# Optimization experiments

Measured on AMD Instinct MI355X. Metric: run time of the kernel, lower is better.

Reference implementation:

```python
import jax, jax.numpy as jnp
import numpy as np

N_NODES = 100000
D_NODE = 80
N_EDGES = 1600000


def setup_inputs() -> dict:
    key = jax.random.key(0)
    ks = jax.random.split(key, 8)
    nodeEmbed = jax.random.normal(ks[0], (N_NODES, D_NODE), dtype=jnp.float32)
    edge_index = jax.random.randint(ks[1], (2, N_EDGES), 0, N_NODES, dtype=jnp.int32)
    # Linear params (fan-in scaled)
    W1 = jax.random.normal(ks[2], (161, 32), dtype=jnp.float32) / np.sqrt(161.0)
    b1 = jax.random.normal(ks[3], (32,), dtype=jnp.float32) * 0.01
    W2 = jax.random.normal(ks[4], (32, 32), dtype=jnp.float32) / np.sqrt(32.0)
    b2 = jax.random.normal(ks[5], (32,), dtype=jnp.float32) * 0.01
    W3 = jax.random.normal(ks[6], (32, 2), dtype=jnp.float32) / np.sqrt(32.0)
    b3 = jax.random.normal(ks[7], (2,), dtype=jnp.float32) * 0.01
    return {"nodeEmbed": nodeEmbed, "edge_index": edge_index,
            "W1": W1, "b1": b1, "W2": W2, "b2": b2, "W3": W3, "b3": b3}


def reference(nodeEmbed, edge_index, W1, b1, W2, b2, W3, b3):
    # embedEdges: gather src/dst node embeddings, concat with constant edge feat
    x_src = nodeEmbed[edge_index[0]]          # [E, 80]
    x_dst = nodeEmbed[edge_index[1]]          # [E, 80]
    edge_feats = jnp.ones((edge_index.shape[1], 1), dtype=nodeEmbed.dtype)
    edge_embed = jnp.concatenate([x_src, edge_feats, x_dst], axis=-1)  # [E, 161]
    # forward: lin1 -> relu -> lin2 -> relu -> lin3 -> log_softmax
    h = jax.nn.relu(edge_embed @ W1 + b1)     # [E, 32]
    h = jax.nn.relu(h @ W2 + b2)              # [E, 32]
    logits = h @ W3 + b3                      # [E, 2]
    return jax.nn.log_softmax(logits, axis=1)
```

## Files before the change

### kernel.cpp

```cpp
#include <hip/hip_runtime.h>
#include <hip/hip_bf16.h>

#define D_NODE 80
#define EDGE_ITERS 8

typedef __attribute__((ext_vector_type(8))) short short8;
typedef __attribute__((ext_vector_type(16))) float f32x16;

__device__ __forceinline__ float bf16lo(unsigned u) {
    return __uint_as_float(u << 16);
}
__device__ __forceinline__ float bf16hi(unsigned u) {
    return __uint_as_float(u & 0xffff0000u);
}
__device__ __forceinline__ unsigned packbf2(float a, float b) {
    __hip_bfloat162 h = __float22bfloat162_rn(make_float2(a, b));
    union { __hip_bfloat162 h2; unsigned u; } cv; cv.h2 = h;
    return cv.u;
}
__device__ __forceinline__ short f2bf(float f) {
    __hip_bfloat16 h = __float2bfloat16(f);
    union { __hip_bfloat16 h1; short s; } cv; cv.h1 = h;
    return cv.s;
}

__global__ __launch_bounds__(256) void proj_kernel(
    const float* __restrict__ X, const float* __restrict__ W1,
    const float* __restrict__ b1,
    unsigned short* __restrict__ PS, unsigned short* __restrict__ PD, int N)
{
    const int lane = threadIdx.x & 63;
    const int wave = threadIdx.x >> 6;
    const int n    = lane & 31;
    const int hi   = lane >> 5;

    short8 Ws[5], Wd[5];
#pragma unroll
    for (int s = 0; s < 5; ++s) {
#pragma unroll
        for (int j = 0; j < 8; ++j) {
            int k = s * 16 + hi * 8 + j;
            Ws[s][j] = f2bf(W1[k * 32 + n]);
            Wd[s][j] = f2bf(W1[(81 + k) * 32 + n]);
        }
    }
    float cdInit[16];
#pragma unroll
    for (int r = 0; r < 16; ++r) {
        int f = (r & 3) + 8 * (r >> 2) + 4 * hi;
        cdInit[r] = b1[f] + W1[80 * 32 + f];
    }

    const int tiles = N / 32;
    for (int tile = blockIdx.x * 4 + wave; tile < tiles; tile += gridDim.x * 4) {
        const int node = tile * 32 + n;
        const float4* xrow = (const float4*)(X + (size_t)node * D_NODE + hi * 8);

        f32x16 cs, cd;
#pragma unroll
        for (int r = 0; r < 16; ++r) { cs[r] = 0.0f; cd[r] = cdInit[r]; }

#pragma unroll
        for (int s = 0; s < 5; ++s) {
            float4 xa = xrow[s * 4];
            float4 xb = xrow[s * 4 + 1];
            union { uint4 u; short8 s8; } Bx;
            Bx.u.x = packbf2(xa.x, xa.y);
            Bx.u.y = packbf2(xa.z, xa.w);
            Bx.u.z = packbf2(xb.x, xb.y);
            Bx.u.w = packbf2(xb.z, xb.w);
            cs = __builtin_amdgcn_mfma_f32_32x32x16_bf16(Ws[s], Bx.s8, cs, 0, 0, 0);
            cd = __builtin_amdgcn_mfma_f32_32x32x16_bf16(Wd[s], Bx.s8, cd, 0, 0, 0);
        }

        unsigned short* psr = PS + (size_t)node * 32 + hi * 4;
        unsigned short* pdr = PD + (size_t)node * 32 + hi * 4;
#pragma unroll
        for (int q = 0; q < 4; ++q) {
            uint2 vs = make_uint2(packbf2(cs[4*q+0], cs[4*q+1]),
                                  packbf2(cs[4*q+2], cs[4*q+3]));
            uint2 vd = make_uint2(packbf2(cd[4*q+0], cd[4*q+1]),
                                  packbf2(cd[4*q+2], cd[4*q+3]));
            *(uint2*)(psr + q * 8) = vs;
            *(uint2*)(pdr + q * 8) = vd;
        }
    }
}

__global__ __launch_bounds__(256) void edge_kernel(
    const int* __restrict__ ei,
    const unsigned short* __restrict__ PS, const unsigned short* __restrict__ PD,
    const float* __restrict__ W2, const float* __restrict__ b2,
    const float* __restrict__ W3, const float* __restrict__ b3,
    float* __restrict__ out, int E)
{
    const int tid  = threadIdx.x;
    const int wave = tid >> 6;
    const int lane = tid & 63;
    const int n    = lane & 31;
    const int hi   = lane >> 5;

    short8 Wa0, Wa1;
#pragma unroll
    for (int j = 0; j < 8; ++j) {
        int k0 = hi * 8 + j;
        Wa0[j] = f2bf(W2[k0 * 32 + n]);
        Wa1[j] = f2bf(W2[(16 + k0) * 32 + n]);
    }
    unsigned b2p[8], w3p[16];
#pragma unroll
    for (int r = 0; r < 16; ++r) {
        int row = (r & 3) + 8 * (r >> 2) + 4 * hi;
        w3p[r] = packbf2(W3[row * 2 + 0], W3[row * 2 + 1]);
        if ((r & 1) == 0) {
            int row2 = ((r + 1) & 3) + 8 * ((r + 1) >> 2) + 4 * hi;
            b2p[r >> 1] = packbf2(b2[row], b2[row2]);
        }
    }
    const float b30 = b3[0], b31 = b3[1];

    const long base = ((long)blockIdx.x * 4 + wave) * (32 * EDGE_ITERS);

    int sIdx[EDGE_ITERS], dIdx[EDGE_ITERS];
#pragma unroll
    for (int it = 0; it < EDGE_ITERS; ++it) {
        long e = base + (long)it * 32 + n;
        int ec = (e < E) ? (int)e : 0;
        sIdx[it] = ei[ec];
        dIdx[it] = ei[(size_t)E + ec];
    }

    uint4 av0 = *(const uint4*)(PS + (size_t)sIdx[0] * 32 + hi * 8);
    uint4 av1 = *(const uint4*)(PS + (size_t)sIdx[0] * 32 + 16 + hi * 8);
    uint4 bv0 = *(const uint4*)(PD + (size_t)dIdx[0] * 32 + hi * 8);
    uint4 bv1 = *(const uint4*)(PD + (size_t)dIdx[0] * 32 + 16 + hi * 8);

#pragma unroll
    for (int it = 0; it < EDGE_ITERS; ++it) {
        uint4 pav0, pav1, pbv0, pbv1;
        if (it + 1 < EDGE_ITERS) {
            pav0 = *(const uint4*)(PS + (size_t)sIdx[it+1] * 32 + hi * 8);
            pav1 = *(const uint4*)(PS + (size_t)sIdx[it+1] * 32 + 16 + hi * 8);
            pbv0 = *(const uint4*)(PD + (size_t)dIdx[it+1] * 32 + hi * 8);
            pbv1 = *(const uint4*)(PD + (size_t)dIdx[it+1] * 32 + 16 + hi * 8);
        }

        union { uint4 u; short8 s8; } B0, B1;
        B0.u.x = packbf2(fmaxf(bf16lo(av0.x) + bf16lo(bv0.x), 0.f),
                         fmaxf(bf16hi(av0.x) + bf16hi(bv0.x), 0.f));
        B0.u.y = packbf2(fmaxf(bf16lo(av0.y) + bf16lo(bv0.y), 0.f),
                         fmaxf(bf16hi(av0.y) + bf16hi(bv0.y), 0.f));
        B0.u.z = packbf2(fmaxf(bf16lo(av0.z) + bf16lo(bv0.z), 0.f),
                         fmaxf(bf16hi(av0.z) + bf16hi(bv0.z), 0.f));
        B0.u.w = packbf2(fmaxf(bf16lo(av0.w) + bf16lo(bv0.w), 0.f),
                         fmaxf(bf16hi(av0.w) + bf16hi(bv0.w), 0.f));
        B1.u.x = packbf2(fmaxf(bf16lo(av1.x) + bf16lo(bv1.x), 0.f),
                         fmaxf(bf16hi(av1.x) + bf16hi(bv1.x), 0.f));
        B1.u.y = packbf2(fmaxf(bf16lo(av1.y) + bf16lo(bv1.y), 0.f),
                         fmaxf(bf16hi(av1.y) + bf16hi(bv1.y), 0.f));
        B1.u.z = packbf2(fmaxf(bf16lo(av1.z) + bf16lo(bv1.z), 0.f),
                         fmaxf(bf16hi(av1.z) + bf16hi(bv1.z), 0.f));
        B1.u.w = packbf2(fmaxf(bf16lo(av1.w) + bf16lo(bv1.w), 0.f),
                         fmaxf(bf16hi(av1.w) + bf16hi(bv1.w), 0.f));

        f32x16 c;
#pragma unroll
        for (int q = 0; q < 8; ++q) {
            c[2*q]   = bf16lo(b2p[q]);
            c[2*q+1] = bf16hi(b2p[q]);
        }
        c = __builtin_amdgcn_mfma_f32_32x32x16_bf16(Wa0, B0.s8, c, 0, 0, 0);
        c = __builtin_amdgcn_mfma_f32_32x32x16_bf16(Wa1, B1.s8, c, 0, 0, 0);

        float p0 = 0.f, p1 = 0.f;
#pragma unroll
        for (int r = 0; r < 16; ++r) {
            float h = fmaxf(c[r], 0.f);
            p0 += h * bf16lo(w3p[r]);
            p1 += h * bf16hi(w3p[r]);
        }
        p0 += __shfl_xor(p0, 32, 64);
        p1 += __shfl_xor(p1, 32, 64);

        if (hi == 0) {
            long eo = base + (long)it * 32 + n;
            if (eo < E) {
                float l0 = p0 + b30;
                float l1 = p1 + b31;
                float mm = fmaxf(l0, l1);
                float z  = __expf(l0 - mm) + __expf(l1 - mm);
                float lse = mm + __logf(z);
                *(float2*)(out + 2 * eo) = make_float2(l0 - lse, l1 - lse);
            }
        }
        av0 = pav0; av1 = pav1; bv0 = pbv0; bv1 = pbv1;
    }
}

extern "C" void kernel_launch(void* const* d_in, const int* in_sizes, int n_in,
                              void* d_out, int out_size, void* d_ws, size_t ws_size,
                              hipStream_t stream) {
    const float* X  = (const float*)d_in[0];
    const int*   ei = (const int*)d_in[1];
    const float* W1 = (const float*)d_in[2];
    const float* b1 = (const float*)d_in[3];
    const float* W2 = (const float*)d_in[4];
    const float* b2 = (const float*)d_in[5];
    const float* W3 = (const float*)d_in[6];
    const float* b3 = (const float*)d_in[7];
    float* out = (float*)d_out;

    int N = in_sizes[0] / D_NODE;
    int E = in_sizes[1] / 2;

    unsigned short* PS = (unsigned short*)d_ws;
    unsigned short* PD = PS + (size_t)N * 32;

    proj_kernel<<<256, 256, 0, stream>>>(X, W1, b1, PS, PD, N);

    int edges_per_block = 4 * 32 * EDGE_ITERS;
    int nblk = (E + edges_per_block - 1) / edges_per_block;
    edge_kernel<<<nblk, 256, 0, stream>>>(ei, PS, PD, W2, b2, W3, b3, out, E);
}
```

Baseline: 67.11 us.

## Issue all edge gathers up front, halve edges per wave, widen projection grid

```diff
diff --git a/kernel.cpp b/kernel.cpp
--- a/kernel.cpp
+++ b/kernel.cpp
@@ -2,7 +2,7 @@
 #include <hip/hip_bf16.h>
 
 #define D_NODE 80
-#define EDGE_ITERS 8
+#define EDGE_ITERS 4
 
 typedef __attribute__((ext_vector_type(8))) short short8;
 typedef __attribute__((ext_vector_type(16))) float f32x16;
@@ -130,38 +130,34 @@
         dIdx[it] = ei[(size_t)E + ec];
     }
 
-    uint4 av0 = *(const uint4*)(PS + (size_t)sIdx[0] * 32 + hi * 8);
-    uint4 av1 = *(const uint4*)(PS + (size_t)sIdx[0] * 32 + 16 + hi * 8);
-    uint4 bv0 = *(const uint4*)(PD + (size_t)dIdx[0] * 32 + hi * 8);
-    uint4 bv1 = *(const uint4*)(PD + (size_t)dIdx[0] * 32 + 16 + hi * 8);
-
+    uint4 av0[EDGE_ITERS], av1[EDGE_ITERS], bv0[EDGE_ITERS], bv1[EDGE_ITERS];
 #pragma unroll
     for (int it = 0; it < EDGE_ITERS; ++it) {
-        uint4 pav0, pav1, pbv0, pbv1;
-        if (it + 1 < EDGE_ITERS) {
-            pav0 = *(const uint4*)(PS + (size_t)sIdx[it+1] * 32 + hi * 8);
-            pav1 = *(const uint4*)(PS + (size_t)sIdx[it+1] * 32 + 16 + hi * 8);
-            pbv0 = *(const uint4*)(PD + (size_t)dIdx[it+1] * 32 + hi * 8);
-            pbv1 = *(const uint4*)(PD + (size_t)dIdx[it+1] * 32 + 16 + hi * 8);
-        }
-
+        av0[it] = *(const uint4*)(PS + (size_t)sIdx[it] * 32 + hi * 8);
+        av1[it] = *(const uint4*)(PS + (size_t)sIdx[it] * 32 + 16 + hi * 8);
+        bv0[it] = *(const uint4*)(PD + (size_t)dIdx[it] * 32 + hi * 8);
+        bv1[it] = *(const uint4*)(PD + (size_t)dIdx[it] * 32 + 16 + hi * 8);
+    }
+
+#pragma unroll
+    for (int it = 0; it < EDGE_ITERS; ++it) {
         union { uint4 u; short8 s8; } B0, B1;
-        B0.u.x = packbf2(fmaxf(bf16lo(av0.x) + bf16lo(bv0.x), 0.f),
-                         fmaxf(bf16hi(av0.x) + bf16hi(bv0.x), 0.f));
-        B0.u.y = packbf2(fmaxf(bf16lo(av0.y) + bf16lo(bv0.y), 0.f),
-                         fmaxf(bf16hi(av0.y) + bf16hi(bv0.y), 0.f));
-        B0.u.z = packbf2(fmaxf(bf16lo(av0.z) + bf16lo(bv0.z), 0.f),
-                         fmaxf(bf16hi(av0.z) + bf16hi(bv0.z), 0.f));
-        B0.u.w = packbf2(fmaxf(bf16lo(av0.w) + bf16lo(bv0.w), 0.f),
-                         fmaxf(bf16hi(av0.w) + bf16hi(bv0.w), 0.f));
-        B1.u.x = packbf2(fmaxf(bf16lo(av1.x) + bf16lo(bv1.x), 0.f),
-                         fmaxf(bf16hi(av1.x) + bf16hi(bv1.x), 0.f));
-        B1.u.y = packbf2(fmaxf(bf16lo(av1.y) + bf16lo(bv1.y), 0.f),
-                         fmaxf(bf16hi(av1.y) + bf16hi(bv1.y), 0.f));
-        B1.u.z = packbf2(fmaxf(bf16lo(av1.z) + bf16lo(bv1.z), 0.f),
-                         fmaxf(bf16hi(av1.z) + bf16hi(bv1.z), 0.f));
-        B1.u.w = packbf2(fmaxf(bf16lo(av1.w) + bf16lo(bv1.w), 0.f),
-                         fmaxf(bf16hi(av1.w) + bf16hi(bv1.w), 0.f));
+        B0.u.x = packbf2(fmaxf(bf16lo(av0[it].x) + bf16lo(bv0[it].x), 0.f),
+                         fmaxf(bf16hi(av0[it].x) + bf16hi(bv0[it].x), 0.f));
+        B0.u.y = packbf2(fmaxf(bf16lo(av0[it].y) + bf16lo(bv0[it].y), 0.f),
+                         fmaxf(bf16hi(av0[it].y) + bf16hi(bv0[it].y), 0.f));
+        B0.u.z = packbf2(fmaxf(bf16lo(av0[it].z) + bf16lo(bv0[it].z), 0.f),
+                         fmaxf(bf16hi(av0[it].z) + bf16hi(bv0[it].z), 0.f));
+        B0.u.w = packbf2(fmaxf(bf16lo(av0[it].w) + bf16lo(bv0[it].w), 0.f),
+                         fmaxf(bf16hi(av0[it].w) + bf16hi(bv0[it].w), 0.f));
+        B1.u.x = packbf2(fmaxf(bf16lo(av1[it].x) + bf16lo(bv1[it].x), 0.f),
+                         fmaxf(bf16hi(av1[it].x) + bf16hi(bv1[it].x), 0.f));
+        B1.u.y = packbf2(fmaxf(bf16lo(av1[it].y) + bf16lo(bv1[it].y), 0.f),
+                         fmaxf(bf16hi(av1[it].y) + bf16hi(bv1[it].y), 0.f));
+        B1.u.z = packbf2(fmaxf(bf16lo(av1[it].z) + bf16lo(bv1[it].z), 0.f),
+                         fmaxf(bf16hi(av1[it].z) + bf16hi(bv1[it].z), 0.f));
+        B1.u.w = packbf2(fmaxf(bf16lo(av1[it].w) + bf16lo(bv1[it].w), 0.f),
+                         fmaxf(bf16hi(av1[it].w) + bf16hi(bv1[it].w), 0.f));
 
         f32x16 c;
 #pragma unroll
@@ -193,7 +189,6 @@
                 *(float2*)(out + 2 * eo) = make_float2(l0 - lse, l1 - lse);
             }
         }
-        av0 = pav0; av1 = pav1; bv0 = pbv0; bv1 = pbv1;
     }
 }
 
@@ -216,7 +211,8 @@
     unsigned short* PS = (unsigned short*)d_ws;
     unsigned short* PD = PS + (size_t)N * 32;
 
-    proj_kernel<<<256, 256, 0, stream>>>(X, W1, b1, PS, PD, N);
+    int ptiles = (N / 32 + 3) / 4;
+    proj_kernel<<<ptiles, 256, 0, stream>>>(X, W1, b1, PS, PD, N);
 
     int edges_per_block = 4 * 32 * EDGE_ITERS;
     int nblk = (E + edges_per_block - 1) / edges_per_block;
```

Result: no change. 66.66 us (-0.7%).
